# Optimization experiments

Hardware: AMD Instinct MI355X
Metric: run time of the kernel (lower is better)

The kernel has to match this reference:

```python
import jax, jax.numpy as jnp
import numpy as np

TAU = 2.0
V_TH = 1.0
SG_ALPHA = 4.0  # spikingjelly surrogate.Sigmoid default

@jax.custom_vjp
def spike_fn(u):
    # heaviside(u) with sigmoid surrogate gradient; u = v - v_threshold
    return (u >= 0.0).astype(u.dtype)

def _spike_fwd(u):
    return spike_fn(u), u

def _spike_bwd(u, g):
    s = jax.nn.sigmoid(SG_ALPHA * u)
    return (g * SG_ALPHA * s * (1.0 - s),)

spike_fn.defvjp(_spike_fwd, _spike_bwd)

def lif_scan(h):
    # h: [T, B, D] input currents; multi-step LIF with hard reset to 0,
    # decay_input=True: v = v + (h - v) / tau
    def step(v, h_t):
        v = v + (h_t - v) / TAU
        s = spike_fn(v - V_TH)
        v = v * (1.0 - jax.lax.stop_gradient(s))  # detach_reset=True, v_reset=0
        return v, s
    v0 = jnp.zeros_like(h[0])
    _, spikes = jax.lax.scan(step, v0, h)
    return spikes  # [T, B, D]

def setup_inputs() -> dict:
    key = jax.random.key(0)
    k_x, k_w1, k_b1, k_w2, k_b2 = jax.random.split(key, 5)
    T, B, D, C = 32, 512, 1024, 1000
    lim1 = 1.0 / np.sqrt(D)
    return {
        "x": jax.random.normal(k_x, (T, B, D), dtype=jnp.float32),
        "W1": jax.random.uniform(k_w1, (D, D), jnp.float32, -lim1, lim1),
        "b1": jax.random.uniform(k_b1, (D,), jnp.float32, -lim1, lim1),
        "W2": jax.random.uniform(k_w2, (C, D), jnp.float32, -lim1, lim1),
        "b2": jax.random.uniform(k_b2, (C,), jnp.float32, -lim1, lim1),
    }

def reference(x, W1, b1, W2, b2):
    # linear_1: [T,B,D] @ [D,D]^T + b1
    h = jnp.einsum('tbd,ed->tbe', x, W1) + b1
    s = lif_scan(h)                               # [T,B,D] spikes in {0,1}
    y = jnp.einsum('tbd,cd->tbc', s, W2) + b2     # [T,B,C]
    y = y.mean(axis=0)                            # [B,C]
    return jax.nn.log_softmax(y, axis=1)
```

## Files before the change

kernel.cpp:

```cpp
#include <hip/hip_runtime.h>
#include <math.h>

#define T_STEPS 32
#define B_SZ    512
#define D_SZ    1024
#define C_SZ    1000
#define KZ      8
#define HP      132

typedef __bf16 bf16x8 __attribute__((ext_vector_type(8)));
typedef float  f32x4  __attribute__((ext_vector_type(4)));

__device__ __forceinline__ unsigned short f2bf(float f) {
    unsigned u = __float_as_uint(f);
    unsigned r = u + 0x7FFFu + ((u >> 16) & 1u);
    return (unsigned short)(r >> 16);
}
__device__ __forceinline__ float bf2f(unsigned short b) {
    return __uint_as_float(((unsigned)b) << 16);
}

__device__ __forceinline__ void async_copy16(const void* g, void* l) {
    __builtin_amdgcn_global_load_lds(
        (const __attribute__((address_space(1))) unsigned int*)g,
        (__attribute__((address_space(3))) unsigned int*)l,
        16, 0, 0);
}

#define NX4  4194304
#define NW14  262144
#define NW24  256000
#define NTOT (NX4 + NW14 + NW24)

__global__ __launch_bounds__(256) void cast_k(
    const float* __restrict__ x,  unsigned short* __restrict__ x_bf,
    const float* __restrict__ W1, unsigned short* __restrict__ W1_bf,
    const float* __restrict__ W2, unsigned short* __restrict__ W2_bf)
{
    const int idx = blockIdx.x * 256 + threadIdx.x;
    if (idx >= NTOT) return;
    const float4* s; ushort4* d; int j;
    if (idx < NX4)              { s = (const float4*)x;  d = (ushort4*)x_bf;  j = idx; }
    else if (idx < NX4 + NW14)  { s = (const float4*)W1; d = (ushort4*)W1_bf; j = idx - NX4; }
    else                        { s = (const float4*)W2; d = (ushort4*)W2_bf; j = idx - NX4 - NW14; }
    const float4 v = s[j];
    ushort4 o;
    o.x = f2bf(v.x); o.y = f2bf(v.y); o.z = f2bf(v.z); o.w = f2bf(v.w);
    d[j] = o;
}

__global__ __launch_bounds__(256) void gemm1_scan_k(
    const unsigned short* __restrict__ A, const unsigned short* __restrict__ Bm,
    const float* __restrict__ bias, unsigned short* __restrict__ cnt)
{
    __shared__ __align__(16) unsigned short smem[128 * HP];
    unsigned short* As = smem;
    unsigned short* Bs = smem + 8192;

    const int tid  = threadIdx.x;
    const int wave = tid >> 6;
    const int lane = tid & 63;
    const int lm   = lane & 15;
    const int quad = lane >> 4;
    const int wm   = (wave >> 1) * 64;
    const int wn   = (wave & 1) * 64;

    const int f  = blockIdx.x;
    const int yb = f & 127;
    const int xb = f >> 7;
    const int b0 = yb * 4;
    const int n0 = xb * 128;

    f32x4 acc[4][4];
    #pragma unroll
    for (int i = 0; i < 4; ++i)
        #pragma unroll
        for (int j = 0; j < 4; ++j)
            acc[i][j] = (f32x4){0.f, 0.f, 0.f, 0.f};

    int srow[4], sgq[4];
    size_t arowoff[4];
    unsigned ldsoff[4];
    #pragma unroll
    for (int p = 0; p < 4; ++p) {
        const int s = p * 256 + tid;
        const int rho = s >> 3;
        srow[p] = rho;
        sgq[p]  = (s & 7) ^ (rho & 7);
        arowoff[p] = (size_t)((rho >> 2) * 512 + b0 + (rho & 3)) * D_SZ;
        ldsoff[p] = (unsigned)(p * 256 + wave * 64) * 16u;
    }
    const int fq0 = quad ^ (lm & 7);

    for (int k0 = 0; k0 < D_SZ; k0 += 64) {
        #pragma unroll
        for (int p = 0; p < 4; ++p) {
            async_copy16(A + arowoff[p] + k0 + sgq[p] * 8, (char*)As + ldsoff[p]);
            async_copy16(Bm + (size_t)(n0 + srow[p]) * D_SZ + k0 + sgq[p] * 8,
                         (char*)Bs + ldsoff[p]);
        }
        __syncthreads();

        #pragma unroll
        for (int kk = 0; kk < 2; ++kk) {
            const int fqk = fq0 ^ (kk * 4);
            bf16x8 af[4], bfr[4];
            #pragma unroll
            for (int i = 0; i < 4; ++i) {
                af[i]  = ((const bf16x8*)As)[(wm + i * 16 + lm) * 8 + fqk];
                bfr[i] = ((const bf16x8*)Bs)[(wn + i * 16 + lm) * 8 + fqk];
            }
            #pragma unroll
            for (int mi = 0; mi < 4; ++mi)
                #pragma unroll
                for (int ni = 0; ni < 4; ++ni)
                    acc[mi][ni] = __builtin_amdgcn_mfma_f32_16x16x32_bf16(
                        af[mi], bfr[ni], acc[mi][ni], 0, 0, 0);
        }
        __syncthreads();
    }

    #pragma unroll
    for (int ni = 0; ni < 4; ++ni) {
        const int nn = wn + ni * 16 + lm;
        const float bv = bias[n0 + nn];
        #pragma unroll
        for (int mi = 0; mi < 4; ++mi) {
            const f32x4 v = acc[mi][ni];
            #pragma unroll
            for (int r = 0; r < 4; ++r)
                smem[(wm + mi * 16 + quad * 4 + r) * HP + nn] = f2bf(v[r] + bv);
        }
    }
    __syncthreads();

    #pragma unroll
    for (int rep = 0; rep < 2; ++rep) {
        const int flat = rep * 256 + tid;
        const int bb = flat >> 7;
        const int c  = flat & 127;
        float v = 0.f, cv = 0.f;
        #pragma unroll
        for (int t = 0; t < T_STEPS; ++t) {
            const float ht = bf2f(smem[(t * 4 + bb) * HP + c]);
            v = 0.5f * (v + ht);
            const float s = (v >= 1.0f) ? 1.0f : 0.0f;
            cv += s;
            v *= (1.0f - s);
        }
        cnt[(size_t)(b0 + bb) * D_SZ + n0 + c] = f2bf(cv);
    }
}

__global__ __launch_bounds__(256) void gemm2_splitk_k(
    const unsigned short* __restrict__ A, const unsigned short* __restrict__ Bm,
    float* __restrict__ partial)
{
    __shared__ __align__(16) unsigned short As[128 * 32];
    __shared__ __align__(16) unsigned short Bs[128 * 32];

    const int tid  = threadIdx.x;
    const int wave = tid >> 6;
    const int lane = tid & 63;
    const int lm   = lane & 15;
    const int quad = lane >> 4;
    const int wm   = (wave >> 1) * 64;
    const int wn   = (wave & 1) * 64;
    const int n0   = blockIdx.x * 128;
    const int m0   = blockIdx.y * 128;
    const int kz   = blockIdx.z;

    f32x4 acc[4][4];
    #pragma unroll
    for (int i = 0; i < 4; ++i)
        #pragma unroll
        for (int j = 0; j < 4; ++j)
            acc[i][j] = (f32x4){0.f, 0.f, 0.f, 0.f};

    int srow[2], sgq[2];
    unsigned ldsoff[2];
    #pragma unroll
    for (int p = 0; p < 2; ++p) {
        const int s = p * 256 + tid;
        srow[p] = s >> 2;
        sgq[p]  = (s & 3) ^ ((srow[p] >> 1) & 3);
        ldsoff[p] = (unsigned)(p * 256 + wave * 64) * 16u;
    }
    const int fq = quad ^ ((lm >> 1) & 3);

    const int kbeg = kz * (D_SZ / KZ);
    for (int k0 = kbeg; k0 < kbeg + D_SZ / KZ; k0 += 32) {
        #pragma unroll
        for (int p = 0; p < 2; ++p) {
            async_copy16(A + (size_t)(m0 + srow[p]) * D_SZ + k0 + sgq[p] * 8,
                         (char*)As + ldsoff[p]);
            int brow = n0 + srow[p];
            if (brow > C_SZ - 1) brow = C_SZ - 1;
            async_copy16(Bm + (size_t)brow * D_SZ + k0 + sgq[p] * 8,
                         (char*)Bs + ldsoff[p]);
        }
        __syncthreads();

        bf16x8 af[4], bfr[4];
        #pragma unroll
        for (int i = 0; i < 4; ++i) {
            af[i]  = ((const bf16x8*)As)[(wm + i * 16 + lm) * 4 + fq];
            bfr[i] = ((const bf16x8*)Bs)[(wn + i * 16 + lm) * 4 + fq];
        }
        #pragma unroll
        for (int mi = 0; mi < 4; ++mi)
            #pragma unroll
            for (int ni = 0; ni < 4; ++ni)
                acc[mi][ni] = __builtin_amdgcn_mfma_f32_16x16x32_bf16(
                    af[mi], bfr[ni], acc[mi][ni], 0, 0, 0);
        __syncthreads();
    }

    #pragma unroll
    for (int ni = 0; ni < 4; ++ni) {
        const int nn = n0 + wn + ni * 16 + lm;
        if (nn >= C_SZ) continue;
        #pragma unroll
        for (int mi = 0; mi < 4; ++mi) {
            const f32x4 v = acc[mi][ni];
            #pragma unroll
            for (int r = 0; r < 4; ++r) {
                const int mm = m0 + wm + mi * 16 + quad * 4 + r;
                partial[((size_t)kz * B_SZ + mm) * C_SZ + nn] = v[r];
            }
        }
    }
}

__global__ __launch_bounds__(256) void reduce_lsm_k(
    const float* __restrict__ partial, const float* __restrict__ b2,
    float* __restrict__ out)
{
    __shared__ float red_max[4];
    __shared__ float red_sum[4];

    const int b   = blockIdx.x;
    const int tid = threadIdx.x;

    float vals[4];
    float m = -1e30f;
    #pragma unroll
    for (int k = 0; k < 4; ++k) {
        const int c = tid + k * 256;
        if (c < C_SZ) {
            float s = 0.f;
            #pragma unroll
            for (int z = 0; z < KZ; ++z)
                s += partial[((size_t)z * B_SZ + b) * C_SZ + c];
            vals[k] = s * (1.0f / (float)T_STEPS) + b2[c];
        } else {
            vals[k] = -1e30f;
        }
        m = fmaxf(m, vals[k]);
    }
    #pragma unroll
    for (int off = 32; off > 0; off >>= 1)
        m = fmaxf(m, __shfl_down(m, off, 64));
    const int wave = tid >> 6;
    const int lane = tid & 63;
    if (lane == 0) red_max[wave] = m;
    __syncthreads();
    m = fmaxf(fmaxf(red_max[0], red_max[1]), fmaxf(red_max[2], red_max[3]));

    float s = 0.f;
    #pragma unroll
    for (int k = 0; k < 4; ++k) {
        const int c = tid + k * 256;
        if (c < C_SZ) s += __expf(vals[k] - m);
    }
    #pragma unroll
    for (int off = 32; off > 0; off >>= 1)
        s += __shfl_down(s, off, 64);
    if (lane == 0) red_sum[wave] = s;
    __syncthreads();
    s = red_sum[0] + red_sum[1] + red_sum[2] + red_sum[3];

    const float lse = m + logf(s);
    #pragma unroll
    for (int k = 0; k < 4; ++k) {
        const int c = tid + k * 256;
        if (c < C_SZ) out[(size_t)b * C_SZ + c] = vals[k] - lse;
    }
}

extern "C" void kernel_launch(void* const* d_in, const int* in_sizes, int n_in,
                              void* d_out, int out_size, void* d_ws, size_t ws_size,
                              hipStream_t stream)
{
    const float* x  = (const float*)d_in[0];
    const float* W1 = (const float*)d_in[1];
    const float* b1 = (const float*)d_in[2];
    const float* W2 = (const float*)d_in[3];
    const float* b2 = (const float*)d_in[4];
    float* out = (float*)d_out;

    char* ws = (char*)d_ws;
    unsigned short* x_bf    = (unsigned short*)(ws);
    unsigned short* W1_bf   = (unsigned short*)(ws + 33554432);
    unsigned short* W2_bf   = (unsigned short*)(ws + 35651584);
    unsigned short* cnt_bf  = (unsigned short*)(ws + 37699584);
    float*          partial = (float*)(ws + 38748160);

    cast_k<<<(NTOT + 255) / 256, 256, 0, stream>>>(
        x, x_bf, W1, W1_bf, W2, W2_bf);

    gemm1_scan_k<<<(B_SZ / 4) * (D_SZ / 128), 256, 0, stream>>>(
        x_bf, W1_bf, b1, cnt_bf);

    {
        dim3 grid((C_SZ + 127) / 128, B_SZ / 128, KZ);
        gemm2_splitk_k<<<grid, 256, 0, stream>>>(cnt_bf, W2_bf, partial);
    }

    reduce_lsm_k<<<B_SZ, 256, 0, stream>>>(partial, b2, out);
}
```

Before: 164.5 us.

## Fuse x fp32-to-bf16 cast into GEMM1 register loads and vectorize scan

```diff
diff --git a/kernel.cpp b/kernel.cpp
--- a/kernel.cpp
+++ b/kernel.cpp
@@ -27,22 +27,25 @@
         16, 0, 0);
 }
 
-#define NX4  4194304
+__device__ __forceinline__ bf16x8 cvt8(const float4 u, const float4 v) {
+    bf16x8 r;
+    r[0] = (__bf16)u.x; r[1] = (__bf16)u.y; r[2] = (__bf16)u.z; r[3] = (__bf16)u.w;
+    r[4] = (__bf16)v.x; r[5] = (__bf16)v.y; r[6] = (__bf16)v.z; r[7] = (__bf16)v.w;
+    return r;
+}
+
 #define NW14  262144
 #define NW24  256000
-#define NTOT (NX4 + NW14 + NW24)
-
-__global__ __launch_bounds__(256) void cast_k(
-    const float* __restrict__ x,  unsigned short* __restrict__ x_bf,
+#define NWTOT (NW14 + NW24)
+
+__global__ __launch_bounds__(256) void cast_w_k(
     const float* __restrict__ W1, unsigned short* __restrict__ W1_bf,
     const float* __restrict__ W2, unsigned short* __restrict__ W2_bf)
 {
     const int idx = blockIdx.x * 256 + threadIdx.x;
-    if (idx >= NTOT) return;
     const float4* s; ushort4* d; int j;
-    if (idx < NX4)              { s = (const float4*)x;  d = (ushort4*)x_bf;  j = idx; }
-    else if (idx < NX4 + NW14)  { s = (const float4*)W1; d = (ushort4*)W1_bf; j = idx - NX4; }
-    else                        { s = (const float4*)W2; d = (ushort4*)W2_bf; j = idx - NX4 - NW14; }
+    if (idx < NW14) { s = (const float4*)W1; d = (ushort4*)W1_bf; j = idx; }
+    else            { s = (const float4*)W2; d = (ushort4*)W2_bf; j = idx - NW14; }
     const float4 v = s[j];
     ushort4 o;
     o.x = f2bf(v.x); o.y = f2bf(v.y); o.z = f2bf(v.z); o.w = f2bf(v.w);
@@ -50,12 +53,11 @@
 }
 
 __global__ __launch_bounds__(256) void gemm1_scan_k(
-    const unsigned short* __restrict__ A, const unsigned short* __restrict__ Bm,
+    const float* __restrict__ X, const unsigned short* __restrict__ Bm,
     const float* __restrict__ bias, unsigned short* __restrict__ cnt)
 {
     __shared__ __align__(16) unsigned short smem[128 * HP];
-    unsigned short* As = smem;
-    unsigned short* Bs = smem + 8192;
+    unsigned short* Bs = smem;
 
     const int tid  = threadIdx.x;
     const int wave = tid >> 6;
@@ -79,7 +81,6 @@
             acc[i][j] = (f32x4){0.f, 0.f, 0.f, 0.f};
 
     int srow[4], sgq[4];
-    size_t arowoff[4];
     unsigned ldsoff[4];
     #pragma unroll
     for (int p = 0; p < 4; ++p) {
@@ -87,28 +88,43 @@
         const int rho = s >> 3;
         srow[p] = rho;
         sgq[p]  = (s & 7) ^ (rho & 7);
-        arowoff[p] = (size_t)((rho >> 2) * 512 + b0 + (rho & 3)) * D_SZ;
         ldsoff[p] = (unsigned)(p * 256 + wave * 64) * 16u;
     }
     const int fq0 = quad ^ (lm & 7);
 
+    const float* arow[4];
+    #pragma unroll
+    for (int i = 0; i < 4; ++i) {
+        const int rho = wm + i * 16 + lm;
+        arow[i] = X + (size_t)((rho >> 2) * 512 + b0 + (rho & 3)) * D_SZ + quad * 8;
+    }
+
     for (int k0 = 0; k0 < D_SZ; k0 += 64) {
         #pragma unroll
-        for (int p = 0; p < 4; ++p) {
-            async_copy16(A + arowoff[p] + k0 + sgq[p] * 8, (char*)As + ldsoff[p]);
+        for (int p = 0; p < 4; ++p)
             async_copy16(Bm + (size_t)(n0 + srow[p]) * D_SZ + k0 + sgq[p] * 8,
                          (char*)Bs + ldsoff[p]);
+        float4 a0[4][2];
+        #pragma unroll
+        for (int i = 0; i < 4; ++i) {
+            a0[i][0] = *(const float4*)(arow[i] + k0);
+            a0[i][1] = *(const float4*)(arow[i] + k0 + 4);
         }
         __syncthreads();
 
-        #pragma unroll
-        for (int kk = 0; kk < 2; ++kk) {
-            const int fqk = fq0 ^ (kk * 4);
-            bf16x8 af[4], bfr[4];
+        {
+            bf16x8 bfr[4], af[4];
+            #pragma unroll
+            for (int i = 0; i < 4; ++i)
+                bfr[i] = ((const bf16x8*)Bs)[(wn + i * 16 + lm) * 8 + fq0];
+            #pragma unroll
+            for (int i = 0; i < 4; ++i)
+                af[i] = cvt8(a0[i][0], a0[i][1]);
+            float4 a1[4][2];
             #pragma unroll
             for (int i = 0; i < 4; ++i) {
-                af[i]  = ((const bf16x8*)As)[(wm + i * 16 + lm) * 8 + fqk];
-                bfr[i] = ((const bf16x8*)Bs)[(wn + i * 16 + lm) * 8 + fqk];
+                a1[i][0] = *(const float4*)(arow[i] + k0 + 32);
+                a1[i][1] = *(const float4*)(arow[i] + k0 + 36);
             }
             #pragma unroll
             for (int mi = 0; mi < 4; ++mi)
@@ -116,6 +132,19 @@
                 for (int ni = 0; ni < 4; ++ni)
                     acc[mi][ni] = __builtin_amdgcn_mfma_f32_16x16x32_bf16(
                         af[mi], bfr[ni], acc[mi][ni], 0, 0, 0);
+            bf16x8 bfr1[4], af1[4];
+            #pragma unroll
+            for (int i = 0; i < 4; ++i)
+                bfr1[i] = ((const bf16x8*)Bs)[(wn + i * 16 + lm) * 8 + (fq0 ^ 4)];
+            #pragma unroll
+            for (int i = 0; i < 4; ++i)
+                af1[i] = cvt8(a1[i][0], a1[i][1]);
+            #pragma unroll
+            for (int mi = 0; mi < 4; ++mi)
+                #pragma unroll
+                for (int ni = 0; ni < 4; ++ni)
+                    acc[mi][ni] = __builtin_amdgcn_mfma_f32_16x16x32_bf16(
+                        af1[mi], bfr1[ni], acc[mi][ni], 0, 0, 0);
         }
         __syncthreads();
     }
@@ -134,21 +163,26 @@
     }
     __syncthreads();
 
-    #pragma unroll
-    for (int rep = 0; rep < 2; ++rep) {
-        const int flat = rep * 256 + tid;
-        const int bb = flat >> 7;
-        const int c  = flat & 127;
-        float v = 0.f, cv = 0.f;
+    {
+        const unsigned* smemU = (const unsigned*)smem;
+        const int bb = tid >> 6;
+        const int c2 = tid & 63;
+        float v0 = 0.f, cv0 = 0.f, v1 = 0.f, cv1 = 0.f;
         #pragma unroll
         for (int t = 0; t < T_STEPS; ++t) {
-            const float ht = bf2f(smem[(t * 4 + bb) * HP + c]);
-            v = 0.5f * (v + ht);
-            const float s = (v >= 1.0f) ? 1.0f : 0.0f;
-            cv += s;
-            v *= (1.0f - s);
-        }
-        cnt[(size_t)(b0 + bb) * D_SZ + n0 + c] = f2bf(cv);
+            const unsigned u = smemU[(t * 4 + bb) * (HP / 2) + c2];
+            const float h0 = bf2f((unsigned short)(u & 0xFFFFu));
+            const float h1 = bf2f((unsigned short)(u >> 16));
+            v0 = 0.5f * (v0 + h0);
+            const float s0 = (v0 >= 1.0f) ? 1.0f : 0.0f;
+            cv0 += s0; v0 *= (1.0f - s0);
+            v1 = 0.5f * (v1 + h1);
+            const float s1 = (v1 >= 1.0f) ? 1.0f : 0.0f;
+            cv1 += s1; v1 *= (1.0f - s1);
+        }
+        ushort2 o;
+        o.x = f2bf(cv0); o.y = f2bf(cv1);
+        *(ushort2*)&cnt[(size_t)(b0 + bb) * D_SZ + n0 + 2 * c2] = o;
     }
 }
 
@@ -300,17 +334,15 @@
     float* out = (float*)d_out;
 
     char* ws = (char*)d_ws;
-    unsigned short* x_bf    = (unsigned short*)(ws);
-    unsigned short* W1_bf   = (unsigned short*)(ws + 33554432);
-    unsigned short* W2_bf   = (unsigned short*)(ws + 35651584);
-    unsigned short* cnt_bf  = (unsigned short*)(ws + 37699584);
-    float*          partial = (float*)(ws + 38748160);
-
-    cast_k<<<(NTOT + 255) / 256, 256, 0, stream>>>(
-        x, x_bf, W1, W1_bf, W2, W2_bf);
+    unsigned short* W1_bf   = (unsigned short*)(ws);
+    unsigned short* W2_bf   = (unsigned short*)(ws + 2097152);
+    unsigned short* cnt_bf  = (unsigned short*)(ws + 4145152);
+    float*          partial = (float*)(ws + 5193728);
+
+    cast_w_k<<<NWTOT / 256, 256, 0, stream>>>(W1, W1_bf, W2, W2_bf);
 
     gemm1_scan_k<<<(B_SZ / 4) * (D_SZ / 128), 256, 0, stream>>>(
-        x_bf, W1_bf, b1, cnt_bf);
+        x, W1_bf, b1, cnt_bf);
 
     {
         dim3 grid((C_SZ + 127) / 128, B_SZ / 128, KZ);
```

Result: slower. 237.4 us (+44.4%).

## Double-buffer GEMM1 K-loop with async LDS prefetch and vectorize LIF scan

Applied to the files above, without the earlier changes.

```diff
diff --git a/kernel.cpp b/kernel.cpp
--- a/kernel.cpp
+++ b/kernel.cpp
@@ -54,8 +54,6 @@
     const float* __restrict__ bias, unsigned short* __restrict__ cnt)
 {
     __shared__ __align__(16) unsigned short smem[128 * HP];
-    unsigned short* As = smem;
-    unsigned short* Bs = smem + 8192;
 
     const int tid  = threadIdx.x;
     const int wave = tid >> 6;
@@ -78,47 +76,54 @@
         for (int j = 0; j < 4; ++j)
             acc[i][j] = (f32x4){0.f, 0.f, 0.f, 0.f};
 
-    int srow[4], sgq[4];
-    size_t arowoff[4];
-    unsigned ldsoff[4];
-    #pragma unroll
-    for (int p = 0; p < 4; ++p) {
+    const unsigned short* asrc[2];
+    const unsigned short* bsrc[2];
+    unsigned dstoff[2];
+    #pragma unroll
+    for (int p = 0; p < 2; ++p) {
         const int s = p * 256 + tid;
-        const int rho = s >> 3;
-        srow[p] = rho;
-        sgq[p]  = (s & 7) ^ (rho & 7);
-        arowoff[p] = (size_t)((rho >> 2) * 512 + b0 + (rho & 3)) * D_SZ;
-        ldsoff[p] = (unsigned)(p * 256 + wave * 64) * 16u;
-    }
-    const int fq0 = quad ^ (lm & 7);
-
-    for (int k0 = 0; k0 < D_SZ; k0 += 64) {
-        #pragma unroll
-        for (int p = 0; p < 4; ++p) {
-            async_copy16(A + arowoff[p] + k0 + sgq[p] * 8, (char*)As + ldsoff[p]);
-            async_copy16(Bm + (size_t)(n0 + srow[p]) * D_SZ + k0 + sgq[p] * 8,
-                         (char*)Bs + ldsoff[p]);
-        }
+        const int row = s >> 2;
+        const int gq = (s & 3) ^ ((row >> 1) & 3);
+        asrc[p] = A + (size_t)((row >> 2) * 512 + b0 + (row & 3)) * D_SZ + gq * 8;
+        bsrc[p] = Bm + (size_t)(n0 + row) * D_SZ + gq * 8;
+        dstoff[p] = (unsigned)(p * 256 + wave * 64) * 16u;
+    }
+    const int fq = quad ^ ((lm >> 1) & 3);
+
+    #pragma unroll
+    for (int p = 0; p < 2; ++p) {
+        async_copy16(asrc[p], (char*)smem + dstoff[p]);
+        async_copy16(bsrc[p], (char*)smem + 8192 + dstoff[p]);
+    }
+
+    for (int it = 0; it < 32; ++it) {
         __syncthreads();
-
-        #pragma unroll
-        for (int kk = 0; kk < 2; ++kk) {
-            const int fqk = fq0 ^ (kk * 4);
-            bf16x8 af[4], bfr[4];
-            #pragma unroll
-            for (int i = 0; i < 4; ++i) {
-                af[i]  = ((const bf16x8*)As)[(wm + i * 16 + lm) * 8 + fqk];
-                bfr[i] = ((const bf16x8*)Bs)[(wn + i * 16 + lm) * 8 + fqk];
+        const int cur = it & 1;
+        if (it + 1 < 32) {
+            const int nb = (cur ^ 1) * 16384;
+            const int k1 = (it + 1) * 32;
+            #pragma unroll
+            for (int p = 0; p < 2; ++p) {
+                async_copy16(asrc[p] + k1, (char*)smem + nb + dstoff[p]);
+                async_copy16(bsrc[p] + k1, (char*)smem + nb + 8192 + dstoff[p]);
             }
-            #pragma unroll
-            for (int mi = 0; mi < 4; ++mi)
-                #pragma unroll
-                for (int ni = 0; ni < 4; ++ni)
-                    acc[mi][ni] = __builtin_amdgcn_mfma_f32_16x16x32_bf16(
-                        af[mi], bfr[ni], acc[mi][ni], 0, 0, 0);
-        }
-        __syncthreads();
-    }
+        }
+        const unsigned short* As = smem + cur * 8192;
+        const unsigned short* Bs = As + 4096;
+        bf16x8 af[4], bfr[4];
+        #pragma unroll
+        for (int i = 0; i < 4; ++i) {
+            af[i]  = ((const bf16x8*)As)[(wm + i * 16 + lm) * 4 + fq];
+            bfr[i] = ((const bf16x8*)Bs)[(wn + i * 16 + lm) * 4 + fq];
+        }
+        #pragma unroll
+        for (int mi = 0; mi < 4; ++mi)
+            #pragma unroll
+            for (int ni = 0; ni < 4; ++ni)
+                acc[mi][ni] = __builtin_amdgcn_mfma_f32_16x16x32_bf16(
+                    af[mi], bfr[ni], acc[mi][ni], 0, 0, 0);
+    }
+    __syncthreads();
 
     #pragma unroll
     for (int ni = 0; ni < 4; ++ni) {
@@ -134,21 +139,26 @@
     }
     __syncthreads();
 
-    #pragma unroll
-    for (int rep = 0; rep < 2; ++rep) {
-        const int flat = rep * 256 + tid;
-        const int bb = flat >> 7;
-        const int c  = flat & 127;
-        float v = 0.f, cv = 0.f;
+    {
+        const unsigned* smemU = (const unsigned*)smem;
+        const int bb = tid >> 6;
+        const int c2 = tid & 63;
+        float v0 = 0.f, cv0 = 0.f, v1 = 0.f, cv1 = 0.f;
         #pragma unroll
         for (int t = 0; t < T_STEPS; ++t) {
-            const float ht = bf2f(smem[(t * 4 + bb) * HP + c]);
-            v = 0.5f * (v + ht);
-            const float s = (v >= 1.0f) ? 1.0f : 0.0f;
-            cv += s;
-            v *= (1.0f - s);
-        }
-        cnt[(size_t)(b0 + bb) * D_SZ + n0 + c] = f2bf(cv);
+            const unsigned u = smemU[(t * 4 + bb) * (HP / 2) + c2];
+            const float h0 = bf2f((unsigned short)(u & 0xFFFFu));
+            const float h1 = bf2f((unsigned short)(u >> 16));
+            v0 = 0.5f * (v0 + h0);
+            const float s0 = (v0 >= 1.0f) ? 1.0f : 0.0f;
+            cv0 += s0; v0 *= (1.0f - s0);
+            v1 = 0.5f * (v1 + h1);
+            const float s1 = (v1 >= 1.0f) ? 1.0f : 0.0f;
+            cv1 += s1; v1 *= (1.0f - s1);
+        }
+        ushort2 o;
+        o.x = f2bf(cv0); o.y = f2bf(cv1);
+        *(ushort2*)&cnt[(size_t)(b0 + bb) * D_SZ + n0 + 2 * c2] = o;
     }
 }
 
```

Result: slower. 176.9 us (+7.5%).
